# Kernel tuning notes

Measured on AMD Instinct MI355X. Metric: run time of the kernel, lower is better.

## Reference

```python
import jax, jax.numpy as jnp
import numpy as np

N, C_IN, H, W = 32, 16, 256, 256
C_OUT, K = 64, 3

def setup_inputs() -> dict:
    key = jax.random.key(0)
    kx, kw, kb = jax.random.split(key, 3)
    x = jax.random.normal(kx, (N, C_IN, H, W), dtype=jnp.float32)
    # PyTorch Conv2d default init: U(-b, b), b = 1/sqrt(fan_in)
    bound = 1.0 / np.sqrt(C_IN * K * K)
    conv_weight = jax.random.uniform(kw, (C_OUT, C_IN, K, K), minval=-bound, maxval=bound, dtype=jnp.float32)
    conv_bias = jax.random.uniform(kb, (C_OUT,), minval=-bound, maxval=bound, dtype=jnp.float32)
    return {"x": x, "conv_weight": conv_weight, "conv_bias": conv_bias}

def reference(x, conv_weight, conv_bias):
    # conv2d, stride=1, padding=0 (VALID), NCHW / OIHW
    y = jax.lax.conv_general_dilated(
        x, conv_weight,
        window_strides=(1, 1), padding="VALID",
        dimension_numbers=("NCHW", "OIHW", "NCHW"))
    y = y + conv_bias[None, :, None, None]
    # min over output channels (keepdim -> 1 channel), then double tanh
    y = jnp.min(y, axis=1, keepdims=True)  # [N,1,OH,OW]
    return jnp.tanh(jnp.tanh(y))
```

## Files before the change

kernel.cpp:

```cpp
#include <hip/hip_runtime.h>

typedef __bf16 bf16x8 __attribute__((ext_vector_type(8)));
typedef unsigned short us8 __attribute__((ext_vector_type(8)));
typedef unsigned short us2 __attribute__((ext_vector_type(2)));
typedef float f32x16 __attribute__((ext_vector_type(16)));

#define N_IMG 32
#define CI 16
#define HH 256
#define WW 256
#define CO 64
#define OHH 254
#define OWW 254
#define RPB 2
#define NBLK_H (OHH / RPB)

#define XS_W 258
#define XS_C 24
#define WP_SHORTS (CO * 160)
#define WS_NEEDED ((size_t)WP_SHORTS * 2)

__device__ __forceinline__ unsigned short f2bf(float f) {
  union { float f; unsigned u; } v; v.f = f;
  return (unsigned short)((v.u + 0x7FFFu + ((v.u >> 16) & 1u)) >> 16);
}

#if defined(__has_builtin)
#if __has_builtin(__builtin_amdgcn_cvt_pk_bf16_f32)
#define HAVE_CVT_PK 1
#endif
#endif

__device__ __forceinline__ us2 cvt2(float a, float b) {
#ifdef HAVE_CVT_PK
  typedef __bf16 bf16x2 __attribute__((ext_vector_type(2)));
  bf16x2 r = __builtin_amdgcn_cvt_pk_bf16_f32(a, b);
  return __builtin_bit_cast(us2, r);
#else
  us2 r; r[0] = f2bf(a); r[1] = f2bf(b); return r;
#endif
}

__device__ __forceinline__ float fast_tanh(float x) {
  float cx = fminf(fmaxf(x, -15.f), 15.f);
  float e = __expf(2.f * cx);
  return (e - 1.f) / (e + 1.f);
}

__global__ void prep_w(const float* __restrict__ wg, const float* __restrict__ bg,
                       unsigned short* __restrict__ wp) {
  int idx = blockIdx.x * 256 + threadIdx.x;
  if (idx >= WP_SHORTS) return;
  int oc = idx / 160;
  int k = idx - oc * 160;
  int tap = k >> 4, ci = k & 15;
  float v;
  if (tap < 9)      v = wg[oc * 144 + ci * 9 + tap];
  else if (ci == 0) v = bg[oc];
  else              v = 0.f;
  wp[idx] = f2bf(v);
}

__global__ __launch_bounds__(256, 2)
void conv_fused(const float* __restrict__ xg, const unsigned short* __restrict__ wp,
                float* __restrict__ out) {
  __shared__ __align__(16) unsigned short xs[(RPB + 2) * XS_W * XS_C];
  const int t = threadIdx.x;
  const int n = blockIdx.x / NBLK_H;
  const int oh0 = (blockIdx.x % NBLK_H) * RPB;

  {
    const float* src = xg + (size_t)n * (CI * HH * WW) + t;
#pragma unroll
    for (int r = 0; r < RPB + 2; ++r) {
#pragma unroll
      for (int h = 0; h < 2; ++h) {
        float v[8];
#pragma unroll
        for (int j = 0; j < 8; ++j)
          v[j] = src[((size_t)(h * 8 + j) * HH + (oh0 + r)) * WW];
        union { us8 v8; us2 v2[4]; } pk;
#pragma unroll
        for (int j = 0; j < 4; ++j) pk.v2[j] = cvt2(v[2 * j], v[2 * j + 1]);
        *(us8*)(xs + ((r * XS_W) + t) * XS_C + h * 8) = pk.v8;
      }
    }
  }
  if (t < 32 * (RPB + 2)) {
    int r = t >> 5, rem = t & 31;
    int w = 256 + (rem >> 4), ci = rem & 15;
    xs[(r * XS_W + w) * XS_C + ci] = 0;
  }
  __syncthreads();

  const int lane = t & 63, wave = t >> 6;
  const int lr = lane & 31, qh = lane >> 5;

  const unsigned short* wpl = wp + lr * 160 + qh * 8;
  bf16x8 afrag[2][10];
#pragma unroll
  for (int mt = 0; mt < 2; ++mt)
#pragma unroll
    for (int tap = 0; tap < 10; ++tap)
      afrag[mt][tap] =
          __builtin_bit_cast(bf16x8, *(const us8*)(wpl + mt * 32 * 160 + tap * 16));

  us8 onev = {};
  if (qh == 0) onev[0] = 0x3F80;
  const bf16x8 xone = __builtin_bit_cast(bf16x8, onev);

  const int pb = wave * 64;

#pragma unroll
  for (int r = 0; r < RPB; ++r) {
    f32x16 acc[2][2];
#pragma unroll
    for (int a = 0; a < 2; ++a)
#pragma unroll
      for (int b = 0; b < 2; ++b)
#pragma unroll
        for (int e = 0; e < 16; ++e) acc[a][b][e] = 0.f;

#pragma unroll
    for (int tap = 0; tap < 9; ++tap) {
      const int kh = tap / 3, kw = tap - kh * 3;
#pragma unroll
      for (int nt = 0; nt < 2; ++nt) {
        bf16x8 xf = __builtin_bit_cast(
            bf16x8,
            *(const us8*)(xs + ((r + kh) * XS_W + pb + nt * 32 + lr + kw) * XS_C +
                          qh * 8));
        acc[0][nt] = __builtin_amdgcn_mfma_f32_32x32x16_bf16(afrag[0][tap], xf,
                                                             acc[0][nt], 0, 0, 0);
        acc[1][nt] = __builtin_amdgcn_mfma_f32_32x32x16_bf16(afrag[1][tap], xf,
                                                             acc[1][nt], 0, 0, 0);
      }
    }
#pragma unroll
    for (int nt = 0; nt < 2; ++nt) {
      acc[0][nt] = __builtin_amdgcn_mfma_f32_32x32x16_bf16(afrag[0][9], xone,
                                                           acc[0][nt], 0, 0, 0);
      acc[1][nt] = __builtin_amdgcn_mfma_f32_32x32x16_bf16(afrag[1][9], xone,
                                                           acc[1][nt], 0, 0, 0);
    }

    float vmin[2];
#pragma unroll
    for (int nt = 0; nt < 2; ++nt) {
      float v = acc[0][nt][0];
#pragma unroll
      for (int e = 1; e < 16; ++e) v = fminf(v, acc[0][nt][e]);
#pragma unroll
      for (int e = 0; e < 16; ++e) v = fminf(v, acc[1][nt][e]);
      v = fminf(v, __shfl_xor(v, 32, 64));
      vmin[nt] = fast_tanh(fast_tanh(v));
    }
    float res = (lane < 32) ? vmin[0] : vmin[1];
    int ow = pb + lane;
    if (ow < OWW) out[((size_t)n * OHH + (oh0 + r)) * OWW + ow] = res;
  }
}

#define WS_K 168
__global__ __launch_bounds__(256, 2)
void conv_min_tanh(const float* __restrict__ xg, const float* __restrict__ wg,
                   const float* __restrict__ bg, float* __restrict__ out) {
  __shared__ __align__(16) unsigned short xs[3 * XS_W * XS_C];
  __shared__ __align__(16) unsigned short ws[CO * WS_K];
  const int t = threadIdx.x;
  const int n = blockIdx.x / OHH;
  const int oh = blockIdx.x % OHH;
#pragma unroll
  for (int i = 0; i < 36; ++i) {
    int f = i * 256 + t;
    int oc = f / 144;
    int r = f - oc * 144;
    int ci = r / 9;
    int tap = r - ci * 9;
    ws[oc * WS_K + tap * 16 + ci] = f2bf(wg[f]);
  }
  if (t < CO) ws[t * WS_K + 144] = f2bf(bg[t]);
  for (int i = t; i < CO * 15; i += 256) {
    int oc = i / 15;
    ws[oc * WS_K + 145 + (i - oc * 15)] = 0;
  }
  {
    const size_t base_n = (size_t)n * CI * HH * WW;
#pragma unroll
    for (int kh = 0; kh < 3; ++kh) {
#pragma unroll
      for (int half = 0; half < 2; ++half) {
        float v[8];
#pragma unroll
        for (int j = 0; j < 8; ++j) {
          int ci = half * 8 + j;
          v[j] = xg[base_n + ((size_t)ci * HH + (oh + kh)) * WW + t];
        }
        us8 pk;
#pragma unroll
        for (int j = 0; j < 8; ++j) pk[j] = f2bf(v[j]);
        *(us8*)(xs + (kh * XS_W + t) * XS_C + half * 8) = pk;
      }
    }
  }
  if (t < 96) {
    int kh = t >> 5;
    int rem = t & 31;
    int w = 256 + (rem >> 4);
    int ci = rem & 15;
    xs[(kh * XS_W + w) * XS_C + ci] = 0;
  }
  __syncthreads();
  const int lane = t & 63, wave = t >> 6;
  const int lr = lane & 31, qh = lane >> 5;
  bf16x8 afrag[2][10];
#pragma unroll
  for (int mt = 0; mt < 2; ++mt) {
    const unsigned short* wq = ws + (mt * 32 + lr) * WS_K + qh * 8;
#pragma unroll
    for (int tap = 0; tap < 10; ++tap)
      afrag[mt][tap] = __builtin_bit_cast(bf16x8, *(const us8*)(wq + tap * 16));
  }
  f32x16 acc[2][2];
#pragma unroll
  for (int a = 0; a < 2; ++a)
#pragma unroll
    for (int b = 0; b < 2; ++b)
#pragma unroll
      for (int e = 0; e < 16; ++e) acc[a][b][e] = 0.f;
  const unsigned short* xq = xs + (wave * 64 + lr) * XS_C + qh * 8;
#pragma unroll
  for (int tap = 0; tap < 9; ++tap) {
    const int kh = tap / 3, kw = tap - kh * 3;
#pragma unroll
    for (int nt = 0; nt < 2; ++nt) {
      bf16x8 xf = __builtin_bit_cast(
          bf16x8, *(const us8*)(xq + (kh * XS_W + nt * 32 + kw) * XS_C));
      acc[0][nt] = __builtin_amdgcn_mfma_f32_32x32x16_bf16(afrag[0][tap], xf,
                                                           acc[0][nt], 0, 0, 0);
      acc[1][nt] = __builtin_amdgcn_mfma_f32_32x32x16_bf16(afrag[1][tap], xf,
                                                           acc[1][nt], 0, 0, 0);
    }
  }
  {
    us8 one = {};
    if (qh == 0) one[0] = 0x3F80;
    bf16x8 xone = __builtin_bit_cast(bf16x8, one);
#pragma unroll
    for (int nt = 0; nt < 2; ++nt) {
      acc[0][nt] = __builtin_amdgcn_mfma_f32_32x32x16_bf16(afrag[0][9], xone,
                                                           acc[0][nt], 0, 0, 0);
      acc[1][nt] = __builtin_amdgcn_mfma_f32_32x32x16_bf16(afrag[1][9], xone,
                                                           acc[1][nt], 0, 0, 0);
    }
  }
  float vmin[2];
#pragma unroll
  for (int nt = 0; nt < 2; ++nt) {
    float v = acc[0][nt][0];
#pragma unroll
    for (int e = 1; e < 16; ++e) v = fminf(v, acc[0][nt][e]);
#pragma unroll
    for (int e = 0; e < 16; ++e) v = fminf(v, acc[1][nt][e]);
    v = fminf(v, __shfl_xor(v, 32, 64));
    vmin[nt] = fast_tanh(fast_tanh(v));
  }
  float res = (lane < 32) ? vmin[0] : vmin[1];
  int ow = wave * 64 + lane;
  if (ow < OWW) out[((size_t)n * OHH + oh) * OWW + ow] = res;
}

extern "C" void kernel_launch(void* const* d_in, const int* in_sizes, int n_in,
                              void* d_out, int out_size, void* d_ws, size_t ws_size,
                              hipStream_t stream) {
  const float* x = (const float*)d_in[0];
  const float* w = (const float*)d_in[1];
  const float* b = (const float*)d_in[2];
  float* out = (float*)d_out;
  if (ws_size >= WS_NEEDED) {
    unsigned short* wp = (unsigned short*)d_ws;
    prep_w<<<dim3((WP_SHORTS + 255) / 256), dim3(256), 0, stream>>>(w, b, wp);
    conv_fused<<<dim3(N_IMG * NBLK_H), dim3(256), 0, stream>>>(x, wp, out);
  } else {
    conv_min_tanh<<<dim3(N_IMG * OHH), dim3(256), 0, stream>>>(x, w, b, out);
  }
}
```

Before: 214.8 us.

## Remap blocks per XCD, reload weight fragments per tap, raise occupancy

Block indices are remapped so that each XCD processes a contiguous range of work items, which keeps neighbouring row blocks of the same image on one L2. Weight A-fragments are no longer held in registers for the whole kernel; they are reloaded from global/L1 at each tap. This frees VGPRs so launch bounds can request 3 blocks per SM. The staging load now issues all 16 channel loads of a row together. The trade-off is extra weight loads inside the inner loop in return for more waves and better L2 locality.

Result: slower. 227.7 us (+6.0%).

```diff
diff --git a/kernel.cpp b/kernel.cpp
--- a/kernel.cpp
+++ b/kernel.cpp
@@ -14,6 +14,8 @@
 #define OWW 254
 #define RPB 2
 #define NBLK_H (OHH / RPB)
+#define NBLK (N_IMG * NBLK_H)
+#define BLK_PER_XCD (NBLK / 8)
 
 #define XS_W 258
 #define XS_C 24
@@ -61,29 +63,28 @@
   wp[idx] = f2bf(v);
 }
 
-__global__ __launch_bounds__(256, 2)
+__global__ __launch_bounds__(256, 3)
 void conv_fused(const float* __restrict__ xg, const unsigned short* __restrict__ wp,
                 float* __restrict__ out) {
   __shared__ __align__(16) unsigned short xs[(RPB + 2) * XS_W * XS_C];
   const int t = threadIdx.x;
-  const int n = blockIdx.x / NBLK_H;
-  const int oh0 = (blockIdx.x % NBLK_H) * RPB;
+  const int work = (blockIdx.x & 7) * BLK_PER_XCD + (blockIdx.x >> 3);
+  const int n = work / NBLK_H;
+  const int oh0 = (work - n * NBLK_H) * RPB;
 
   {
     const float* src = xg + (size_t)n * (CI * HH * WW) + t;
 #pragma unroll
     for (int r = 0; r < RPB + 2; ++r) {
-#pragma unroll
-      for (int h = 0; h < 2; ++h) {
-        float v[8];
-#pragma unroll
-        for (int j = 0; j < 8; ++j)
-          v[j] = src[((size_t)(h * 8 + j) * HH + (oh0 + r)) * WW];
-        union { us8 v8; us2 v2[4]; } pk;
-#pragma unroll
-        for (int j = 0; j < 4; ++j) pk.v2[j] = cvt2(v[2 * j], v[2 * j + 1]);
-        *(us8*)(xs + ((r * XS_W) + t) * XS_C + h * 8) = pk.v8;
-      }
+      float v[16];
+#pragma unroll
+      for (int j = 0; j < 16; ++j)
+        v[j] = src[((size_t)j * HH + (oh0 + r)) * WW];
+      union { us8 v8[2]; us2 v2[8]; } pk;
+#pragma unroll
+      for (int j = 0; j < 8; ++j) pk.v2[j] = cvt2(v[2 * j], v[2 * j + 1]);
+      *(us8*)(xs + (r * XS_W + t) * XS_C) = pk.v8[0];
+      *(us8*)(xs + (r * XS_W + t) * XS_C + 8) = pk.v8[1];
     }
   }
   if (t < 32 * (RPB + 2)) {
@@ -95,15 +96,7 @@
 
   const int lane = t & 63, wave = t >> 6;
   const int lr = lane & 31, qh = lane >> 5;
-
   const unsigned short* wpl = wp + lr * 160 + qh * 8;
-  bf16x8 afrag[2][10];
-#pragma unroll
-  for (int mt = 0; mt < 2; ++mt)
-#pragma unroll
-    for (int tap = 0; tap < 10; ++tap)
-      afrag[mt][tap] =
-          __builtin_bit_cast(bf16x8, *(const us8*)(wpl + mt * 32 * 160 + tap * 16));
 
   us8 onev = {};
   if (qh == 0) onev[0] = 0x3F80;
@@ -124,24 +117,32 @@
 #pragma unroll
     for (int tap = 0; tap < 9; ++tap) {
       const int kh = tap / 3, kw = tap - kh * 3;
+      bf16x8 af0 = __builtin_bit_cast(bf16x8, *(const us8*)(wpl + tap * 16));
+      bf16x8 af1 =
+          __builtin_bit_cast(bf16x8, *(const us8*)(wpl + 32 * 160 + tap * 16));
 #pragma unroll
       for (int nt = 0; nt < 2; ++nt) {
         bf16x8 xf = __builtin_bit_cast(
             bf16x8,
             *(const us8*)(xs + ((r + kh) * XS_W + pb + nt * 32 + lr + kw) * XS_C +
                           qh * 8));
-        acc[0][nt] = __builtin_amdgcn_mfma_f32_32x32x16_bf16(afrag[0][tap], xf,
+        acc[0][nt] = __builtin_amdgcn_mfma_f32_32x32x16_bf16(af0, xf,
                                                              acc[0][nt], 0, 0, 0);
-        acc[1][nt] = __builtin_amdgcn_mfma_f32_32x32x16_bf16(afrag[1][tap], xf,
+        acc[1][nt] = __builtin_amdgcn_mfma_f32_32x32x16_bf16(af1, xf,
                                                              acc[1][nt], 0, 0, 0);
       }
     }
-#pragma unroll
-    for (int nt = 0; nt < 2; ++nt) {
-      acc[0][nt] = __builtin_amdgcn_mfma_f32_32x32x16_bf16(afrag[0][9], xone,
-                                                           acc[0][nt], 0, 0, 0);
-      acc[1][nt] = __builtin_amdgcn_mfma_f32_32x32x16_bf16(afrag[1][9], xone,
-                                                           acc[1][nt], 0, 0, 0);
+    {
+      bf16x8 af0 = __builtin_bit_cast(bf16x8, *(const us8*)(wpl + 9 * 16));
+      bf16x8 af1 =
+          __builtin_bit_cast(bf16x8, *(const us8*)(wpl + 32 * 160 + 9 * 16));
+#pragma unroll
+      for (int nt = 0; nt < 2; ++nt) {
+        acc[0][nt] = __builtin_amdgcn_mfma_f32_32x32x16_bf16(af0, xone,
+                                                             acc[0][nt], 0, 0, 0);
+        acc[1][nt] = __builtin_amdgcn_mfma_f32_32x32x16_bf16(af1, xone,
+                                                             acc[1][nt], 0, 0, 0);
+      }
     }
 
     float vmin[2];
@@ -280,7 +281,7 @@
   if (ws_size >= WS_NEEDED) {
     unsigned short* wp = (unsigned short*)d_ws;
     prep_w<<<dim3((WP_SHORTS + 255) / 256), dim3(256), 0, stream>>>(w, b, wp);
-    conv_fused<<<dim3(N_IMG * NBLK_H), dim3(256), 0, stream>>>(x, wp, out);
+    conv_fused<<<dim3(NBLK), dim3(256), 0, stream>>>(x, wp, out);
   } else {
     conv_min_tanh<<<dim3(N_IMG * OHH), dim3(256), 0, stream>>>(x, w, b, out);
   }
```
